# Performance work log

Measured on AMD Instinct MI355X. Metric: run time of the kernel, lower is better.

## Reference

```python
import jax, jax.numpy as jnp
import numpy as np

B, T, D, H, FF, TB = 4, 512, 768, 12, 3072, 64
DK = D // H
E = float(np.e)
NEG = -1e9  # stand-in for float('-inf') masked_fill; rows always have valid entries


def layer_norm(x, g, b, eps=1e-5):
    m = jnp.mean(x, axis=-1, keepdims=True)
    v = jnp.mean((x - m) ** 2, axis=-1, keepdims=True)
    return (x - m) * jax.lax.rsqrt(v + eps) * g + b


def setup_inputs() -> dict:
    key = jax.random.key(0)
    ks = jax.random.split(key, 20)
    s = 0.02
    w = lambda k, shape: jax.random.normal(k, shape, jnp.float32) * s
    return {
        "x": jax.random.normal(ks[0], (B, T, D), jnp.float32),
        "batch_temporal_mat": jax.random.uniform(ks[1], (B, T, T), jnp.float32, 0.0, 100.0),
        "padding_masks": jnp.ones((B, 1, T, T), jnp.int32),
        # attention linears (stored (in,out): y = x @ W + b, equals torch x @ W_t.T + b)
        "wq": w(ks[2], (D, D)), "bq": w(ks[3], (D,)),
        "wk": w(ks[4], (D, D)), "bk": w(ks[5], (D,)),
        "wv": w(ks[6], (D, D)), "bv": w(ks[7], (D,)),
        "wp": w(ks[8], (D, D)), "bp": w(ks[9], (D,)),
        # temporal-bias MLP: Linear(1,TB) -> leaky_relu(0.2) -> Linear(TB,1)
        "tb1_w": w(ks[10], (1, TB)), "tb1_b": w(ks[11], (TB,)),
        "tb2_w": w(ks[12], (TB, 1)), "tb2_b": w(ks[13], (1,)),
        # FFN
        "fc1_w": w(ks[14], (D, FF)), "fc1_b": w(ks[15], (FF,)),
        "fc2_w": w(ks[16], (FF, D)), "fc2_b": w(ks[17], (D,)),
        # layernorms
        "ln1_g": jnp.ones((D,), jnp.float32), "ln1_b": jnp.zeros((D,), jnp.float32),
        "ln2_g": jnp.ones((D,), jnp.float32), "ln2_b": jnp.zeros((D,), jnp.float32),
    }


def _block(x, batch_temporal_mat, padding_masks,
           wq, bq, wk, bk, wv, bv, wp, bp,
           tb1_w, tb1_b, tb2_w, tb2_b,
           fc1_w, fc1_b, fc2_w, fc2_b,
           ln1_g, ln1_b, ln2_g, ln2_b):
    # pre-LN attention sublayer
    h = layer_norm(x, ln1_g, ln1_b)
    q = (h @ wq + bq).reshape(B, T, H, DK).transpose(0, 2, 1, 3)  # (B,H,T,DK)
    k = (h @ wk + bk).reshape(B, T, H, DK).transpose(0, 2, 1, 3)
    v = (h @ wv + bv).reshape(B, T, H, DK).transpose(0, 2, 1, 3)
    scores = jnp.einsum('bhid,bhjd->bhij', q, k) * (DK ** -0.5)  # (B,H,T,T)

    # temporal bias: 1/log(e + dt), then per-(i,j) MLP with leaky_relu(0.2)
    tm = 1.0 / jnp.log(E + batch_temporal_mat)                    # (B,T,T)
    hb = jax.nn.leaky_relu(tm[..., None] @ tb1_w + tb1_b, 0.2)    # (B,T,T,TB)
    bias = (hb @ tb2_w + tb2_b)[..., 0]                           # (B,T,T)
    scores = scores + bias[:, None]

    # padding mask then causal (future) mask with CLS row 0 fully visible
    scores = jnp.where(padding_masks == 0, NEG, scores)
    causal = jnp.triu(jnp.ones((T, T), bool), 1).at[0, :].set(False)
    scores = jnp.where(causal, NEG, scores)

    p = jax.nn.softmax(scores, axis=-1)
    out = jnp.einsum('bhij,bhjd->bhid', p, v).transpose(0, 2, 1, 3).reshape(B, T, D)
    out = out @ wp + bp
    x = x + out

    # pre-LN FFN sublayer (exact GELU as in nn.GELU default)
    h2 = layer_norm(x, ln2_g, ln2_b)
    m = jax.nn.gelu(h2 @ fc1_w + fc1_b, approximate=False) @ fc2_w + fc2_b
    return x + m


def reference(x, batch_temporal_mat, padding_masks,
              wq, bq, wk, bk, wv, bv, wp, bp,
              tb1_w, tb1_b, tb2_w, tb2_b,
              fc1_w, fc1_b, fc2_w, fc2_b,
              ln1_g, ln1_b, ln2_g, ln2_b):
    return _block(x, batch_temporal_mat, padding_masks,
                  wq, bq, wk, bk, wv, bv, wp, bp,
                  tb1_w, tb1_b, tb2_w, tb2_b,
                  fc1_w, fc1_b, fc2_w, fc2_b,
                  ln1_g, ln1_b, ln2_g, ln2_b)
```

## Files before the change

kernel.cpp:

```cpp
#include <hip/hip_runtime.h>
#include <hip/hip_bf16.h>
#include <math.h>

#define B_ 4
#define T_ 512
#define D_ 768
#define H_ 12
#define FF_ 3072
#define DK_ 64
#define NTOK (B_*T_)
#define NEGV -1e9f

typedef unsigned short u16;
typedef __bf16 bfx8 __attribute__((ext_vector_type(8)));
typedef float f32x4 __attribute__((ext_vector_type(4)));
typedef u16 u16x8 __attribute__((ext_vector_type(8)));
typedef u16 u16x4 __attribute__((ext_vector_type(4)));

__device__ __forceinline__ u16 f2bf(float f) {
  union { float f; unsigned u; } v; v.f = f;
  unsigned r = (v.u + 0x7FFFu + ((v.u >> 16) & 1u)) >> 16;
  return (u16)r;
}

__device__ __forceinline__ float bf2f(u16 u) {
  union { unsigned u; float f; } c; c.u = (unsigned)u << 16; return c.f;
}

__device__ __forceinline__ void glds16(const u16* g, u16* l) {
  __builtin_amdgcn_global_load_lds((const __attribute__((address_space(1))) void*)g,
                                   (__attribute__((address_space(3))) void*)l, 16, 0, 0);
}

__global__ __launch_bounds__(256) void prep_kernel(
    const float* __restrict__ x,
    const float* __restrict__ wq, const float* __restrict__ wk,
    const float* __restrict__ wv, const float* __restrict__ wp,
    const float* __restrict__ fc1, const float* __restrict__ fc2,
    u16* wqT, u16* wkT, u16* wvT, u16* wpT, u16* fc1T, u16* fc2T,
    const float* __restrict__ ln1g, const float* __restrict__ ln1b, u16* __restrict__ hbuf,
    const float* __restrict__ tmat, const int* __restrict__ pad,
    const float* __restrict__ tb1w, const float* __restrict__ tb1b,
    const float* __restrict__ tb2w, const float* __restrict__ tb2b,
    float* __restrict__ biasM)
{
  const int bid = blockIdx.x;
  const int tid = threadIdx.x;
  if (bid < 6912) {
    __shared__ float tile[32][33];
    const float* in; u16* outp; int K, N, local;
    if (bid < 2304) {
      int m = bid / 576; local = bid % 576; K = 768; N = 768;
      in   = m == 0 ? wq  : (m == 1 ? wk  : (m == 2 ? wv  : wp));
      outp = m == 0 ? wqT : (m == 1 ? wkT : (m == 2 ? wvT : wpT));
    } else if (bid < 4608) {
      local = bid - 2304; K = 768; N = 3072; in = fc1; outp = fc1T;
    } else {
      local = bid - 4608; K = 3072; N = 768; in = fc2; outp = fc2T;
    }
    const int nt = N / 32;
    const int n0 = (local % nt) * 32, k0 = (local / nt) * 32;
    const int tx = tid & 31, ty = tid >> 5;
    #pragma unroll
    for (int i = 0; i < 4; ++i) {
      int r = ty + i * 8;
      tile[r][tx] = in[(size_t)(k0 + r) * N + n0 + tx];
    }
    __syncthreads();
    const int nloc = tid >> 3;
    const int k4   = (tid & 7) * 4;
    u16x4 vv;
    #pragma unroll
    for (int jj = 0; jj < 4; ++jj) vv[jj] = f2bf(tile[k4 + jj][nloc]);
    *(u16x4*)&outp[(size_t)(n0 + nloc) * K + k0 + k4] = vv;
  } else if (bid < 8960) {
    const int row = bid - 6912;
    const float* xr = x + (size_t)row * D_;
    float v0 = xr[tid], v1 = xr[tid + 256], v2 = xr[tid + 512];
    float s = v0 + v1 + v2;
    float sq = v0 * v0 + v1 * v1 + v2 * v2;
    #pragma unroll
    for (int o = 32; o > 0; o >>= 1) { s += __shfl_down(s, o); sq += __shfl_down(sq, o); }
    __shared__ float ss[4], s2[4];
    int w = tid >> 6;
    if ((tid & 63) == 0) { ss[w] = s; s2[w] = sq; }
    __syncthreads();
    s = ss[0] + ss[1] + ss[2] + ss[3];
    sq = s2[0] + s2[1] + s2[2] + s2[3];
    float mean = s * (1.0f / 768.0f);
    float inv = rsqrtf(sq * (1.0f / 768.0f) - mean * mean + 1e-5f);
    u16* orow = hbuf + (size_t)row * D_;
    orow[tid]       = f2bf((v0 - mean) * inv * ln1g[tid]       + ln1b[tid]);
    orow[tid + 256] = f2bf((v1 - mean) * inv * ln1g[tid + 256] + ln1b[tid + 256]);
    orow[tid + 512] = f2bf((v2 - mean) * inv * ln1g[tid + 512] + ln1b[tid + 512]);
  } else {
    __shared__ float sw1[64], sb1[64], sw2[64];
    if (tid < 64) {
      sw1[tid] = tb1w[tid];
      sb1[tid] = tb1b[tid];
      sw2[tid] = tb2w[tid];
    }
    __syncthreads();
    size_t idx = (size_t)(bid - 8960) * 256 + tid;
    float tm = 1.0f / __logf(2.718281828459045f + tmat[idx]);
    float acc = tb2b[0];
    #pragma unroll
    for (int t = 0; t < 64; ++t) {
      float u = fmaf(tm, sw1[t], sb1[t]);
      u = u > 0.0f ? u : 0.2f * u;
      acc = fmaf(u, sw2[t], acc);
    }
    biasM[idx] = (pad[idx] == 0) ? NEGV : acc;
  }
}

__device__ __forceinline__ void gemm_tile_p2(
    const u16* __restrict__ A, const u16* __restrict__ BT,
    int K, int nk, int m0, int n0, int k0,
    u16* As, u16* Bs, f32x4 acc[4][4])
{
  const int tid = threadIdx.x;
  const int w = tid >> 6, lane = tid & 63;
  const int lr = lane & 15, lk = (lane >> 4) * 8;
  const int wm = (w >> 1) * 64, wn = (w & 1) * 64;
  const int c0 = w * 64 + lane, c1 = 256 + c0;
  const int r0 = c0 >> 2, o0 = (c0 & 3) * 8;
  const int r1 = c1 >> 2, o1 = (c1 & 3) * 8;
  const u16* gA0 = A  + (size_t)(m0 + r0) * K + k0 + o0;
  const u16* gA1 = A  + (size_t)(m0 + r1) * K + k0 + o1;
  const u16* gB0 = BT + (size_t)(n0 + r0) * K + k0 + o0;
  const u16* gB1 = BT + (size_t)(n0 + r1) * K + k0 + o1;
  u16* la0 = As + w * 512;
  u16* la1 = As + 2048 + w * 512;
  u16* lb0 = Bs + w * 512;
  u16* lb1 = Bs + 2048 + w * 512;
#define ISSUE_TILE(kk, b) do { \
    glds16(gA0 + (size_t)(kk) * 32, la0 + (b) * 4096); \
    glds16(gA1 + (size_t)(kk) * 32, la1 + (b) * 4096); \
    glds16(gB0 + (size_t)(kk) * 32, lb0 + (b) * 4096); \
    glds16(gB1 + (size_t)(kk) * 32, lb1 + (b) * 4096); } while (0)
  ISSUE_TILE(0, 0);
  if (nk > 1) ISSUE_TILE(1, 1);
  int cb = 0;
  for (int kt = 0; kt < nk; ++kt) {
    if (kt < nk - 2) asm volatile("s_waitcnt vmcnt(4)" ::: "memory");
    else             asm volatile("s_waitcnt vmcnt(0)" ::: "memory");
    __builtin_amdgcn_sched_barrier(0);
    __builtin_amdgcn_s_barrier();
    __builtin_amdgcn_sched_barrier(0);
    const u16* Asc = As + cb * 4096;
    const u16* Bsc = Bs + cb * 4096;
    bfx8 af[4], bfr[4];
    #pragma unroll
    for (int t = 0; t < 4; ++t) {
      af[t]  = *(const bfx8*)&Asc[(wm + t * 16 + lr) * 32 + lk];
      bfr[t] = *(const bfx8*)&Bsc[(wn + t * 16 + lr) * 32 + lk];
    }
    if (kt + 2 < nk) {
      int nb = cb + 2; if (nb >= 3) nb -= 3;
      ISSUE_TILE(kt + 2, nb);
    }
    #pragma unroll
    for (int rt = 0; rt < 4; ++rt)
      #pragma unroll
      for (int ct = 0; ct < 4; ++ct)
        acc[rt][ct] = __builtin_amdgcn_mfma_f32_16x16x32_bf16(af[rt], bfr[ct], acc[rt][ct], 0, 0, 0);
    cb = cb + 1; if (cb >= 3) cb = 0;
  }
#undef ISSUE_TILE
}

__global__ __launch_bounds__(256) void gemm_qkv(
    const u16* __restrict__ A,
    const u16* __restrict__ wqT, const u16* __restrict__ wkT, const u16* __restrict__ wvT,
    const float* __restrict__ bq, const float* __restrict__ bk, const float* __restrict__ bv,
    u16* __restrict__ qo, u16* __restrict__ ko, u16* __restrict__ vo)
{
  __shared__ u16 As[3 * 128 * 32];
  __shared__ u16 Bs[3 * 128 * 32];
  const int bid = blockIdx.x;
  const int xcd = bid & 7, idx = bid >> 3;
  const int y = xcd * 2 + (idx & 1);
  const int r2 = idx >> 1;
  const int xt = r2 % 6, z = r2 / 6;
  const u16* BT = z == 0 ? wqT : (z == 1 ? wkT : wvT);
  const float* bias = z == 0 ? bq : (z == 1 ? bk : bv);
  u16* outp = z == 0 ? qo : (z == 1 ? ko : vo);
  const float scale = z == 0 ? 0.125f : 1.0f;
  const int m0 = y * 128, n0 = xt * 128;
  f32x4 acc[4][4];
  #pragma unroll
  for (int a = 0; a < 4; ++a)
    #pragma unroll
    for (int bb = 0; bb < 4; ++bb) acc[a][bb] = (f32x4){0.f, 0.f, 0.f, 0.f};
  gemm_tile_p2(A, BT, D_, D_ / 32, m0, n0, 0, As, Bs, acc);
  const int tid = threadIdx.x;
  const int w = tid >> 6, lane = tid & 63;
  const int lr = lane & 15;
  const int wm = (w >> 1) * 64, wn = (w & 1) * 64;
  #pragma unroll
  for (int rt = 0; rt < 4; ++rt)
    #pragma unroll
    for (int ct = 0; ct < 4; ++ct)
      #pragma unroll
      for (int r = 0; r < 4; ++r) {
        int m = m0 + wm + rt * 16 + (lane >> 4) * 4 + r;
        int n = n0 + wn + ct * 16 + lr;
        float val = (acc[rt][ct][r] + bias[n]) * scale;
        int b = m >> 9, t = m & 511, hh = n >> 6, d = n & 63;
        if (z < 2) outp[(((size_t)b * H_ + hh) * T_ + t) * DK_ + d] = f2bf(val);
        else       outp[(((size_t)b * H_ + hh) * DK_ + d) * T_ + t] = f2bf(val);
      }
}

__global__ __launch_bounds__(256) void gemm_part_bf16(
    const u16* __restrict__ A, const u16* __restrict__ BT,
    u16* __restrict__ part, int M, int N, int K, int Ksplit, int nx)
{
  __shared__ u16 As[3 * 128 * 32];
  __shared__ u16 Bs[3 * 128 * 32];
  const int bid = blockIdx.x;
  const int xcd = bid & 7, idx = bid >> 3;
  const int y = xcd * 2 + (idx & 1);
  const int r2 = idx >> 1;
  const int xt = r2 % nx, kz = r2 / nx;
  const int m0 = y * 128, n0 = xt * 128;
  f32x4 acc[4][4];
  #pragma unroll
  for (int a = 0; a < 4; ++a)
    #pragma unroll
    for (int bb = 0; bb < 4; ++bb) acc[a][bb] = (f32x4){0.f, 0.f, 0.f, 0.f};
  gemm_tile_p2(A, BT, K, Ksplit / 32, m0, n0, kz * Ksplit, As, Bs, acc);
  const int tid = threadIdx.x;
  const int w = tid >> 6, lane = tid & 63;
  const int lr = lane & 15;
  const int wm = (w >> 1) * 64, wn = (w & 1) * 64;
  u16* pp = part + (size_t)kz * M * N;
  #pragma unroll
  for (int rt = 0; rt < 4; ++rt)
    #pragma unroll
    for (int ct = 0; ct < 4; ++ct)
      #pragma unroll
      for (int r = 0; r < 4; ++r) {
        int m = m0 + wm + rt * 16 + (lane >> 4) * 4 + r;
        int n = n0 + wn + ct * 16 + lr;
        pp[(size_t)m * N + n] = f2bf(acc[rt][ct][r]);
      }
}

__global__ __launch_bounds__(256) void reduce_ln(
    const u16* __restrict__ part, const float* __restrict__ x, const float* __restrict__ bp,
    const float* __restrict__ g, const float* __restrict__ bta,
    float* __restrict__ x1, u16* __restrict__ h2)
{
  const int row = blockIdx.x;
  const int tid = threadIdx.x;
  const size_t base = (size_t)row * D_;
  const size_t slab = (size_t)NTOK * D_;
  float v[3];
  float s = 0.f, sq = 0.f;
  #pragma unroll
  for (int i = 0; i < 3; ++i) {
    int c = tid + i * 256;
    float val = x[base + c] + bp[c];
    #pragma unroll
    for (int kz = 0; kz < 4; ++kz) val += bf2f(part[kz * slab + base + c]);
    v[i] = val;
    s += val; sq += val * val;
  }
  #pragma unroll
  for (int o = 32; o > 0; o >>= 1) { s += __shfl_down(s, o); sq += __shfl_down(sq, o); }
  __shared__ float ss[4], s2[4];
  int w = tid >> 6;
  if ((tid & 63) == 0) { ss[w] = s; s2[w] = sq; }
  __syncthreads();
  s = ss[0] + ss[1] + ss[2] + ss[3];
  sq = s2[0] + s2[1] + s2[2] + s2[3];
  float mean = s * (1.0f / 768.0f);
  float inv = rsqrtf(sq * (1.0f / 768.0f) - mean * mean + 1e-5f);
  #pragma unroll
  for (int i = 0; i < 3; ++i) {
    int c = tid + i * 256;
    x1[base + c] = v[i];
    h2[base + c] = f2bf((v[i] - mean) * inv * g[c] + bta[c]);
  }
}

__global__ __launch_bounds__(256) void reduce_out(
    const u16* __restrict__ part, const float* __restrict__ x1,
    const float* __restrict__ bias, float* __restrict__ out)
{
  const size_t base = ((size_t)blockIdx.x * 256 + threadIdx.x) * 8;
  const size_t slab = (size_t)NTOK * D_;
  const int nb = (int)(base % D_);
  float s[8];
  float4 a0 = *(const float4*)&x1[base];
  float4 a1 = *(const float4*)&x1[base + 4];
  float4 b0 = *(const float4*)&bias[nb];
  float4 b1 = *(const float4*)&bias[nb + 4];
  s[0] = a0.x + b0.x; s[1] = a0.y + b0.y; s[2] = a0.z + b0.z; s[3] = a0.w + b0.w;
  s[4] = a1.x + b1.x; s[5] = a1.y + b1.y; s[6] = a1.z + b1.z; s[7] = a1.w + b1.w;
  #pragma unroll
  for (int kz = 0; kz < 8; ++kz) {
    u16x8 pv = *(const u16x8*)&part[kz * slab + base];
    #pragma unroll
    for (int j = 0; j < 8; ++j) s[j] += bf2f(pv[j]);
  }
  float4 o0 = {s[0], s[1], s[2], s[3]};
  float4 o1 = {s[4], s[5], s[6], s[7]};
  *(float4*)&out[base]     = o0;
  *(float4*)&out[base + 4] = o1;
}

__global__ __launch_bounds__(256) void gemm_gelu(
    const u16* __restrict__ A, const u16* __restrict__ BT,
    const float* __restrict__ bias, u16* __restrict__ outp, int M, int N, int K)
{
  __shared__ u16 As[3 * 128 * 32];
  __shared__ u16 Bs[3 * 128 * 32];
  const int bid = blockIdx.x;
  const int xcd = bid & 7, idx = bid >> 3;
  const int y = xcd * 2 + (idx & 1);
  const int xt = idx >> 1;
  const int m0 = y * 128, n0 = xt * 128;
  f32x4 acc[4][4];
  #pragma unroll
  for (int a = 0; a < 4; ++a)
    #pragma unroll
    for (int bb = 0; bb < 4; ++bb) acc[a][bb] = (f32x4){0.f, 0.f, 0.f, 0.f};
  gemm_tile_p2(A, BT, K, K / 32, m0, n0, 0, As, Bs, acc);
  const int tid = threadIdx.x;
  const int w = tid >> 6, lane = tid & 63;
  const int lr = lane & 15;
  const int wm = (w >> 1) * 64, wn = (w & 1) * 64;
  #pragma unroll
  for (int rt = 0; rt < 4; ++rt)
    #pragma unroll
    for (int ct = 0; ct < 4; ++ct)
      #pragma unroll
      for (int r = 0; r < 4; ++r) {
        int m = m0 + wm + rt * 16 + (lane >> 4) * 4 + r;
        int n = n0 + wn + ct * 16 + lr;
        float val = acc[rt][ct][r] + bias[n];
        float gl = 0.5f * val * (1.0f + erff(val * 0.7071067811865475f));
        outp[(size_t)m * N + n] = f2bf(gl);
      }
}

__global__ __launch_bounds__(256) void attn_kernel(
    const u16* __restrict__ q, const u16* __restrict__ k, const u16* __restrict__ vT,
    const float* __restrict__ biasM, u16* __restrict__ ao)
{
  __shared__ u16 P[32 * 512];
  __shared__ float pmax[128], psum[128];
  const int tid = threadIdx.x;
  const int w = tid >> 6, lane = tid & 63;
  const int lr = lane & 15, hi = lane >> 4, lk = hi * 8;

  const int bid = blockIdx.x;
  const int xcd = bid & 7, idx = bid >> 3;
  const int bh = xcd * 6 + (idx >> 4);
  const int i0 = (idx & 15) * 32;
  const int b = bh / H_, h = bh % H_;
  const int tmax = (i0 == 0) ? 31 : ((i0 >> 4) + 1);
  const int nks  = (i0 == 0) ? 16 : ((i0 >> 5) + 1);

  bfx8 qf[2][2];
  #pragma unroll
  for (int g = 0; g < 2; ++g)
    #pragma unroll
    for (int ks = 0; ks < 2; ++ks)
      qf[g][ks] = *(const bfx8*)(q + ((size_t)bh * T_ + i0 + g * 16 + lr) * DK_ + ks * 32 + lk);
  f32x4 acc[8][2];
  float mx[2][4];
  #pragma unroll
  for (int g = 0; g < 2; ++g)
    #pragma unroll
    for (int r = 0; r < 4; ++r) mx[g][r] = -3.4e38f;
  #pragma unroll
  for (int ct = 0; ct < 8; ++ct) {
    const int t = ct * 4 + w;
    if (t > tmax) continue;
    const int j0 = t * 16;
    bfx8 kf0 = *(const bfx8*)(k + ((size_t)bh * T_ + j0 + lr) * DK_ + lk);
    bfx8 kf1 = *(const bfx8*)(k + ((size_t)bh * T_ + j0 + lr) * DK_ + 32 + lk);
    const int j = j0 + lr;
    __builtin_amdgcn_s_setprio(1);
    #pragma unroll
    for (int g = 0; g < 2; ++g) {
      f32x4 a0 = (f32x4){0.f, 0.f, 0.f, 0.f};
      a0 = __builtin_amdgcn_mfma_f32_16x16x32_bf16(qf[g][0], kf0, a0, 0, 0, 0);
      a0 = __builtin_amdgcn_mfma_f32_16x16x32_bf16(qf[g][1], kf1, a0, 0, 0, 0);
      acc[ct][g] = a0;
    }
    __builtin_amdgcn_s_setprio(0);
    #pragma unroll
    for (int g = 0; g < 2; ++g)
      #pragma unroll
      for (int r = 0; r < 4; ++r) {
        int i = i0 + g * 16 + hi * 4 + r;
        float s = acc[ct][g][r] + biasM[((size_t)b * T_ + i) * T_ + j];
        if (j > i && i != 0) s = NEGV;
        acc[ct][g][r] = s;
        mx[g][r] = fmaxf(mx[g][r], s);
      }
  }
  #pragma unroll
  for (int o = 1; o < 16; o <<= 1)
    #pragma unroll
    for (int g = 0; g < 2; ++g)
      #pragma unroll
      for (int r = 0; r < 4; ++r) mx[g][r] = fmaxf(mx[g][r], __shfl_xor(mx[g][r], o));
  if (lr == 0) {
    #pragma unroll
    for (int g = 0; g < 2; ++g)
      #pragma unroll
      for (int r = 0; r < 4; ++r) pmax[w * 32 + g * 16 + hi * 4 + r] = mx[g][r];
  }
  __syncthreads();

  float M2[2][4], sm[2][4];
  #pragma unroll
  for (int g = 0; g < 2; ++g)
    #pragma unroll
    for (int r = 0; r < 4; ++r) {
      int row = g * 16 + hi * 4 + r;
      M2[g][r] = fmaxf(fmaxf(pmax[row], pmax[32 + row]), fmaxf(pmax[64 + row], pmax[96 + row]));
      sm[g][r] = 0.f;
    }
  char* Pb = (char*)P;
  #pragma unroll
  for (int ct = 0; ct < 8; ++ct) {
    const int t = ct * 4 + w;
    if (t > tmax) continue;
    const int col = t * 16 + lr;
    #pragma unroll
    for (int g = 0; g < 2; ++g)
      #pragma unroll
      for (int r = 0; r < 4; ++r) {
        float pexp = __expf(acc[ct][g][r] - M2[g][r]);
        sm[g][r] += pexp;
        int row = g * 16 + hi * 4 + r;
        int byte = (row * 1024 + col * 2) ^ ((row & 7) << 4);
        *(u16*)(Pb + byte) = f2bf(pexp);
      }
  }
  #pragma unroll
  for (int o = 1; o < 16; o <<= 1)
    #pragma unroll
    for (int g = 0; g < 2; ++g)
      #pragma unroll
      for (int r = 0; r < 4; ++r) sm[g][r] += __shfl_xor(sm[g][r], o);
  if (lr == 0) {
    #pragma unroll
    for (int g = 0; g < 2; ++g)
      #pragma unroll
      for (int r = 0; r < 4; ++r) psum[w * 32 + g * 16 + hi * 4 + r] = sm[g][r];
  }
  __syncthreads();

  float rinv[2][4];
  #pragma unroll
  for (int g = 0; g < 2; ++g)
    #pragma unroll
    for (int r = 0; r < 4; ++r) {
      int row = g * 16 + hi * 4 + r;
      rinv[g][r] = 1.0f / (psum[row] + psum[32 + row] + psum[64 + row] + psum[96 + row]);
    }

  {
    const int n0 = w * 16;
    f32x4 oa0 = (f32x4){0.f, 0.f, 0.f, 0.f};
    f32x4 oa1 = (f32x4){0.f, 0.f, 0.f, 0.f};
    for (int ks = 0; ks < nks; ++ks) {
      bfx8 vf = *(const bfx8*)(vT + ((size_t)bh * DK_ + n0 + lr) * T_ + ks * 32 + lk);
      int byte0 = (lr * 1024 + (ks * 32 + lk) * 2) ^ ((lr & 7) << 4);
      int byte1 = ((16 + lr) * 1024 + (ks * 32 + lk) * 2) ^ ((lr & 7) << 4);
      bfx8 pa0 = *(const bfx8*)(Pb + byte0);
      bfx8 pa1 = *(const bfx8*)(Pb + byte1);
      __builtin_amdgcn_s_setprio(1);
      oa0 = __builtin_amdgcn_mfma_f32_16x16x32_bf16(pa0, vf, oa0, 0, 0, 0);
      oa1 = __builtin_amdgcn_mfma_f32_16x16x32_bf16(pa1, vf, oa1, 0, 0, 0);
      __builtin_amdgcn_s_setprio(0);
    }
    #pragma unroll
    for (int r = 0; r < 4; ++r) {
      int i = i0 + hi * 4 + r;
      ao[((size_t)b * T_ + i) * D_ + h * DK_ + n0 + lr] = f2bf(oa0[r] * rinv[0][r]);
    }
    #pragma unroll
    for (int r = 0; r < 4; ++r) {
      int i = i0 + 16 + hi * 4 + r;
      ao[((size_t)b * T_ + i) * D_ + h * DK_ + n0 + lr] = f2bf(oa1[r] * rinv[1][r]);
    }
  }
}

extern "C" void kernel_launch(void* const* d_in, const int* in_sizes, int n_in,
                              void* d_out, int out_size, void* d_ws, size_t ws_size,
                              hipStream_t stream) {
  (void)in_sizes; (void)n_in; (void)out_size; (void)ws_size;
  const float* x    = (const float*)d_in[0];
  const float* tmat = (const float*)d_in[1];
  const int*   pad  = (const int*)d_in[2];
  const float* wq = (const float*)d_in[3];  const float* bq = (const float*)d_in[4];
  const float* wk = (const float*)d_in[5];  const float* bk = (const float*)d_in[6];
  const float* wv = (const float*)d_in[7];  const float* bv = (const float*)d_in[8];
  const float* wp = (const float*)d_in[9];  const float* bp = (const float*)d_in[10];
  const float* tb1w = (const float*)d_in[11]; const float* tb1b = (const float*)d_in[12];
  const float* tb2w = (const float*)d_in[13]; const float* tb2b = (const float*)d_in[14];
  const float* fc1w = (const float*)d_in[15]; const float* fc1b = (const float*)d_in[16];
  const float* fc2w = (const float*)d_in[17]; const float* fc2b = (const float*)d_in[18];
  const float* ln1g = (const float*)d_in[19]; const float* ln1b = (const float*)d_in[20];
  const float* ln2g = (const float*)d_in[21]; const float* ln2b = (const float*)d_in[22];
  float* out = (float*)d_out;

  char* p = (char*)d_ws;
  u16* wqT  = (u16*)p; p += (size_t)768 * 768 * 2;
  u16* wkT  = (u16*)p; p += (size_t)768 * 768 * 2;
  u16* wvT  = (u16*)p; p += (size_t)768 * 768 * 2;
  u16* wpT  = (u16*)p; p += (size_t)768 * 768 * 2;
  u16* fc1T = (u16*)p; p += (size_t)768 * 3072 * 2;
  u16* fc2T = (u16*)p; p += (size_t)3072 * 768 * 2;
  float* x1 = (float*)p; p += (size_t)NTOK * D_ * 4;
  u16* gbuf = (u16*)p; p += (size_t)NTOK * FF_ * 2;
  u16* hbuf = (u16*)p; p += (size_t)NTOK * D_ * 2;
  u16* qb   = (u16*)p; p += (size_t)NTOK * D_ * 2;
  u16* kb   = (u16*)p; p += (size_t)NTOK * D_ * 2;
  u16* vTb  = (u16*)p; p += (size_t)NTOK * D_ * 2;
  float* biasM = (float*)p; p += (size_t)B_ * T_ * T_ * 4;
  u16* ao   = (u16*)p; p += (size_t)NTOK * D_ * 2;
  u16* h2   = (u16*)p; p += (size_t)NTOK * D_ * 2;
  u16* partF = (u16*)p; p += (size_t)8 * NTOK * D_ * 2;

  prep_kernel<<<13056, 256, 0, stream>>>(x, wq, wk, wv, wp, fc1w, fc2w,
                                         wqT, wkT, wvT, wpT, fc1T, fc2T,
                                         ln1g, ln1b, hbuf,
                                         tmat, pad, tb1w, tb1b, tb2w, tb2b, biasM);

  gemm_qkv<<<288, 256, 0, stream>>>(hbuf, wqT, wkT, wvT, bq, bk, bv, qb, kb, vTb);
  attn_kernel<<<768, 256, 0, stream>>>(qb, kb, vTb, biasM, ao);

  gemm_part_bf16<<<384, 256, 0, stream>>>(ao, wpT, partF, NTOK, 768, 768, 192, 6);
  reduce_ln<<<NTOK, 256, 0, stream>>>(partF, x, bp, ln2g, ln2b, x1, h2);

  gemm_gelu<<<384, 256, 0, stream>>>(h2, fc1T, fc1b, gbuf, NTOK, FF_, 768);

  gemm_part_bf16<<<768, 256, 0, stream>>>(gbuf, fc2T, partF, NTOK, 768, 3072, 384, 6);
  reduce_out<<<NTOK * D_ / 8 / 256, 256, 0, stream>>>(partF, x1, fc2b, out);
}
```

Baseline: 127.1 us.

## Use 8-wave 512-thread GEMM blocks and a polynomial erf GELU

The GEMM kernels now launch 512 threads (8 waves) per 128x128 tile instead of 4, so each wave computes a 32x64 sub-tile. Each thread issues one A and one B async load per k-step instead of two, and it holds half as many accumulators, which lowers register pressure and adds waves for latency hiding. The fc1 epilogue also swaps erff for an Abramowitz-Stegun polynomial erf approximation with __expf. That is cheaper but slightly less accurate than exact GELU.

```diff
diff --git a/kernel.cpp b/kernel.cpp
--- a/kernel.cpp
+++ b/kernel.cpp
@@ -30,6 +30,16 @@
 __device__ __forceinline__ void glds16(const u16* g, u16* l) {
   __builtin_amdgcn_global_load_lds((const __attribute__((address_space(1))) void*)g,
                                    (__attribute__((address_space(3))) void*)l, 16, 0, 0);
+}
+
+__device__ __forceinline__ float gelu_f(float x) {
+  float ax = fabsf(x) * 0.7071067811865475f;
+  float t = 1.0f / fmaf(0.3275911f, ax, 1.0f);
+  float poly = t * fmaf(t, fmaf(t, fmaf(t, fmaf(t, 1.061405429f, -1.453152027f),
+                                        1.421413741f), -0.284496736f), 0.254829592f);
+  float erfv = 1.0f - poly * __expf(-ax * ax);
+  erfv = x >= 0.f ? erfv : -erfv;
+  return 0.5f * x * (1.0f + erfv);
 }
 
 __global__ __launch_bounds__(256) void prep_kernel(
@@ -114,54 +124,48 @@
   }
 }
 
-__device__ __forceinline__ void gemm_tile_p2(
+__device__ __forceinline__ void gemm_tile_w8(
     const u16* __restrict__ A, const u16* __restrict__ BT,
     int K, int nk, int m0, int n0, int k0,
-    u16* As, u16* Bs, f32x4 acc[4][4])
+    u16* As, u16* Bs, f32x4 acc[2][4])
 {
   const int tid = threadIdx.x;
   const int w = tid >> 6, lane = tid & 63;
   const int lr = lane & 15, lk = (lane >> 4) * 8;
-  const int wm = (w >> 1) * 64, wn = (w & 1) * 64;
-  const int c0 = w * 64 + lane, c1 = 256 + c0;
+  const int wm = (w >> 1) * 32, wn = (w & 1) * 64;
+  const int c0 = w * 64 + lane;
   const int r0 = c0 >> 2, o0 = (c0 & 3) * 8;
-  const int r1 = c1 >> 2, o1 = (c1 & 3) * 8;
-  const u16* gA0 = A  + (size_t)(m0 + r0) * K + k0 + o0;
-  const u16* gA1 = A  + (size_t)(m0 + r1) * K + k0 + o1;
-  const u16* gB0 = BT + (size_t)(n0 + r0) * K + k0 + o0;
-  const u16* gB1 = BT + (size_t)(n0 + r1) * K + k0 + o1;
-  u16* la0 = As + w * 512;
-  u16* la1 = As + 2048 + w * 512;
-  u16* lb0 = Bs + w * 512;
-  u16* lb1 = Bs + 2048 + w * 512;
+  const u16* gA = A  + (size_t)(m0 + r0) * K + k0 + o0;
+  const u16* gB = BT + (size_t)(n0 + r0) * K + k0 + o0;
+  u16* la = As + w * 512;
+  u16* lb = Bs + w * 512;
 #define ISSUE_TILE(kk, b) do { \
-    glds16(gA0 + (size_t)(kk) * 32, la0 + (b) * 4096); \
-    glds16(gA1 + (size_t)(kk) * 32, la1 + (b) * 4096); \
-    glds16(gB0 + (size_t)(kk) * 32, lb0 + (b) * 4096); \
-    glds16(gB1 + (size_t)(kk) * 32, lb1 + (b) * 4096); } while (0)
+    glds16(gA + (size_t)(kk) * 32, la + (b) * 4096); \
+    glds16(gB + (size_t)(kk) * 32, lb + (b) * 4096); } while (0)
   ISSUE_TILE(0, 0);
   if (nk > 1) ISSUE_TILE(1, 1);
   int cb = 0;
   for (int kt = 0; kt < nk; ++kt) {
-    if (kt < nk - 2) asm volatile("s_waitcnt vmcnt(4)" ::: "memory");
+    if (kt < nk - 2) asm volatile("s_waitcnt vmcnt(2)" ::: "memory");
     else             asm volatile("s_waitcnt vmcnt(0)" ::: "memory");
     __builtin_amdgcn_sched_barrier(0);
     __builtin_amdgcn_s_barrier();
     __builtin_amdgcn_sched_barrier(0);
     const u16* Asc = As + cb * 4096;
     const u16* Bsc = Bs + cb * 4096;
-    bfx8 af[4], bfr[4];
-    #pragma unroll
-    for (int t = 0; t < 4; ++t) {
-      af[t]  = *(const bfx8*)&Asc[(wm + t * 16 + lr) * 32 + lk];
+    bfx8 af[2], bfr[4];
+    #pragma unroll
+    for (int t = 0; t < 2; ++t)
+      af[t] = *(const bfx8*)&Asc[(wm + t * 16 + lr) * 32 + lk];
+    #pragma unroll
+    for (int t = 0; t < 4; ++t)
       bfr[t] = *(const bfx8*)&Bsc[(wn + t * 16 + lr) * 32 + lk];
-    }
     if (kt + 2 < nk) {
       int nb = cb + 2; if (nb >= 3) nb -= 3;
       ISSUE_TILE(kt + 2, nb);
     }
     #pragma unroll
-    for (int rt = 0; rt < 4; ++rt)
+    for (int rt = 0; rt < 2; ++rt)
       #pragma unroll
       for (int ct = 0; ct < 4; ++ct)
         acc[rt][ct] = __builtin_amdgcn_mfma_f32_16x16x32_bf16(af[rt], bfr[ct], acc[rt][ct], 0, 0, 0);
@@ -170,7 +174,7 @@
 #undef ISSUE_TILE
 }
 
-__global__ __launch_bounds__(256) void gemm_qkv(
+__global__ __launch_bounds__(512) void gemm_qkv(
     const u16* __restrict__ A,
     const u16* __restrict__ wqT, const u16* __restrict__ wkT, const u16* __restrict__ wvT,
     const float* __restrict__ bq, const float* __restrict__ bk, const float* __restrict__ bv,
@@ -188,23 +192,23 @@
   u16* outp = z == 0 ? qo : (z == 1 ? ko : vo);
   const float scale = z == 0 ? 0.125f : 1.0f;
   const int m0 = y * 128, n0 = xt * 128;
-  f32x4 acc[4][4];
-  #pragma unroll
-  for (int a = 0; a < 4; ++a)
+  f32x4 acc[2][4];
+  #pragma unroll
+  for (int a = 0; a < 2; ++a)
     #pragma unroll
     for (int bb = 0; bb < 4; ++bb) acc[a][bb] = (f32x4){0.f, 0.f, 0.f, 0.f};
-  gemm_tile_p2(A, BT, D_, D_ / 32, m0, n0, 0, As, Bs, acc);
+  gemm_tile_w8(A, BT, D_, D_ / 32, m0, n0, 0, As, Bs, acc);
   const int tid = threadIdx.x;
   const int w = tid >> 6, lane = tid & 63;
-  const int lr = lane & 15;
-  const int wm = (w >> 1) * 64, wn = (w & 1) * 64;
-  #pragma unroll
-  for (int rt = 0; rt < 4; ++rt)
+  const int lr = lane & 15, hi = lane >> 4;
+  const int wm = (w >> 1) * 32, wn = (w & 1) * 64;
+  #pragma unroll
+  for (int rt = 0; rt < 2; ++rt)
     #pragma unroll
     for (int ct = 0; ct < 4; ++ct)
       #pragma unroll
       for (int r = 0; r < 4; ++r) {
-        int m = m0 + wm + rt * 16 + (lane >> 4) * 4 + r;
+        int m = m0 + wm + rt * 16 + hi * 4 + r;
         int n = n0 + wn + ct * 16 + lr;
         float val = (acc[rt][ct][r] + bias[n]) * scale;
         int b = m >> 9, t = m & 511, hh = n >> 6, d = n & 63;
@@ -213,7 +217,7 @@
       }
 }
 
-__global__ __launch_bounds__(256) void gemm_part_bf16(
+__global__ __launch_bounds__(512) void gemm_part_bf16(
     const u16* __restrict__ A, const u16* __restrict__ BT,
     u16* __restrict__ part, int M, int N, int K, int Ksplit, int nx)
 {
@@ -225,24 +229,24 @@
   const int r2 = idx >> 1;
   const int xt = r2 % nx, kz = r2 / nx;
   const int m0 = y * 128, n0 = xt * 128;
-  f32x4 acc[4][4];
-  #pragma unroll
-  for (int a = 0; a < 4; ++a)
+  f32x4 acc[2][4];
+  #pragma unroll
+  for (int a = 0; a < 2; ++a)
     #pragma unroll
     for (int bb = 0; bb < 4; ++bb) acc[a][bb] = (f32x4){0.f, 0.f, 0.f, 0.f};
-  gemm_tile_p2(A, BT, K, Ksplit / 32, m0, n0, kz * Ksplit, As, Bs, acc);
+  gemm_tile_w8(A, BT, K, Ksplit / 32, m0, n0, kz * Ksplit, As, Bs, acc);
   const int tid = threadIdx.x;
   const int w = tid >> 6, lane = tid & 63;
-  const int lr = lane & 15;
-  const int wm = (w >> 1) * 64, wn = (w & 1) * 64;
+  const int lr = lane & 15, hi = lane >> 4;
+  const int wm = (w >> 1) * 32, wn = (w & 1) * 64;
   u16* pp = part + (size_t)kz * M * N;
   #pragma unroll
-  for (int rt = 0; rt < 4; ++rt)
+  for (int rt = 0; rt < 2; ++rt)
     #pragma unroll
     for (int ct = 0; ct < 4; ++ct)
       #pragma unroll
       for (int r = 0; r < 4; ++r) {
-        int m = m0 + wm + rt * 16 + (lane >> 4) * 4 + r;
+        int m = m0 + wm + rt * 16 + hi * 4 + r;
         int n = n0 + wn + ct * 16 + lr;
         pp[(size_t)m * N + n] = f2bf(acc[rt][ct][r]);
       }
@@ -312,7 +316,7 @@
   *(float4*)&out[base + 4] = o1;
 }
 
-__global__ __launch_bounds__(256) void gemm_gelu(
+__global__ __launch_bounds__(512) void gemm_gelu(
     const u16* __restrict__ A, const u16* __restrict__ BT,
     const float* __restrict__ bias, u16* __restrict__ outp, int M, int N, int K)
 {
@@ -323,27 +327,26 @@
   const int y = xcd * 2 + (idx & 1);
   const int xt = idx >> 1;
   const int m0 = y * 128, n0 = xt * 128;
-  f32x4 acc[4][4];
-  #pragma unroll
-  for (int a = 0; a < 4; ++a)
+  f32x4 acc[2][4];
+  #pragma unroll
+  for (int a = 0; a < 2; ++a)
     #pragma unroll
     for (int bb = 0; bb < 4; ++bb) acc[a][bb] = (f32x4){0.f, 0.f, 0.f, 0.f};
-  gemm_tile_p2(A, BT, K, K / 32, m0, n0, 0, As, Bs, acc);
+  gemm_tile_w8(A, BT, K, K / 32, m0, n0, 0, As, Bs, acc);
   const int tid = threadIdx.x;
   const int w = tid >> 6, lane = tid & 63;
-  const int lr = lane & 15;
-  const int wm = (w >> 1) * 64, wn = (w & 1) * 64;
-  #pragma unroll
-  for (int rt = 0; rt < 4; ++rt)
+  const int lr = lane & 15, hi = lane >> 4;
+  const int wm = (w >> 1) * 32, wn = (w & 1) * 64;
+  #pragma unroll
+  for (int rt = 0; rt < 2; ++rt)
     #pragma unroll
     for (int ct = 0; ct < 4; ++ct)
       #pragma unroll
       for (int r = 0; r < 4; ++r) {
-        int m = m0 + wm + rt * 16 + (lane >> 4) * 4 + r;
+        int m = m0 + wm + rt * 16 + hi * 4 + r;
         int n = n0 + wn + ct * 16 + lr;
         float val = acc[rt][ct][r] + bias[n];
-        float gl = 0.5f * val * (1.0f + erff(val * 0.7071067811865475f));
-        outp[(size_t)m * N + n] = f2bf(gl);
+        outp[(size_t)m * N + n] = f2bf(gelu_f(val));
       }
 }
 
@@ -538,14 +541,14 @@
                                          ln1g, ln1b, hbuf,
                                          tmat, pad, tb1w, tb1b, tb2w, tb2b, biasM);
 
-  gemm_qkv<<<288, 256, 0, stream>>>(hbuf, wqT, wkT, wvT, bq, bk, bv, qb, kb, vTb);
+  gemm_qkv<<<288, 512, 0, stream>>>(hbuf, wqT, wkT, wvT, bq, bk, bv, qb, kb, vTb);
   attn_kernel<<<768, 256, 0, stream>>>(qb, kb, vTb, biasM, ao);
 
-  gemm_part_bf16<<<384, 256, 0, stream>>>(ao, wpT, partF, NTOK, 768, 768, 192, 6);
+  gemm_part_bf16<<<384, 512, 0, stream>>>(ao, wpT, partF, NTOK, 768, 768, 192, 6);
   reduce_ln<<<NTOK, 256, 0, stream>>>(partF, x, bp, ln2g, ln2b, x1, h2);
 
-  gemm_gelu<<<384, 256, 0, stream>>>(h2, fc1T, fc1b, gbuf, NTOK, FF_, 768);
-
-  gemm_part_bf16<<<768, 256, 0, stream>>>(gbuf, fc2T, partF, NTOK, 768, 3072, 384, 6);
+  gemm_gelu<<<384, 512, 0, stream>>>(h2, fc1T, fc1b, gbuf, NTOK, FF_, 768);
+
+  gemm_part_bf16<<<768, 512, 0, stream>>>(gbuf, fc2T, partF, NTOK, 768, 3072, 384, 6);
   reduce_out<<<NTOK * D_ / 8 / 256, 256, 0, stream>>>(partF, x1, fc2b, out);
 }
```

Result: no change. 125.5 us (-1.2%).
